# Kernel optimization log

Hardware: AMD Instinct MI355X
Metric: run time of the kernel (lower is better)

## Reference

```python
import jax, jax.numpy as jnp
import numpy as np

COST_CLASS, COST_BBOX, COST_GIOU = 1.0, 5.0, 2.0
BS, Q, K, T = 16, 1024, 256, 128


def setup_inputs() -> dict:
    key = jax.random.key(0)
    k1, k2, k3, k4 = jax.random.split(key, 4)
    pred_logits = jax.random.normal(k1, (BS, Q, K), dtype=jnp.float32)
    # predicted boxes in (mid, width) format, width > 0
    pred_boxes = jax.random.uniform(k2, (BS, Q, 2), dtype=jnp.float32, minval=0.05, maxval=1.0)
    # target boxes in (x0, x1) format with x0 < x1
    tgt_boxes = jnp.sort(jax.random.uniform(k3, (BS, T, 2), dtype=jnp.float32), axis=-1)
    tgt_labels = jax.random.randint(k4, (BS, T), 0, K, dtype=jnp.int32)
    return {"pred_logits": pred_logits, "pred_boxes": pred_boxes,
            "tgt_boxes": tgt_boxes, "tgt_labels": tgt_labels}


def midwtoxy(x):
    mid, w = x[..., 0], x[..., 1]
    return jnp.stack([mid - 0.5 * w, mid + 0.5 * w], axis=-1)


def getgiou(b1, b2):
    # b1: [N,2] (x0,x1), b2: [M,2]; returns [N,M] generalized IoU for 1-D intervals
    area1 = b1[:, 1] - b1[:, 0]              # [N]
    area2 = b2[:, 1] - b2[:, 0]              # [M]
    lt = jnp.maximum(b1[:, None, 0], b2[None, :, 0])
    rb = jnp.minimum(b1[:, None, 1], b2[None, :, 1])
    inter = jnp.clip(rb - lt, 0.0)           # [N,M]
    union = area1[:, None] + area2[None, :] - inter
    iou = inter / union
    hull_lt = jnp.minimum(b1[:, None, 0], b2[None, :, 0])
    hull_rb = jnp.maximum(b1[:, None, 1], b2[None, :, 1])
    hull = jnp.clip(hull_rb - hull_lt, 0.0)
    return iou - (hull - union) / hull


def reference(pred_logits, pred_boxes, tgt_boxes, tgt_labels):
    bs, q, k = pred_logits.shape
    out_prob = jax.nn.softmax(pred_logits.reshape(bs * q, k), axis=-1)  # [bs*Q, K]
    out_bbox = midwtoxy(pred_boxes.reshape(bs * q, 2))                  # [bs*Q, 2] (x0,x1)
    tgt_bbox = tgt_boxes.reshape(-1, 2)                                 # [bs*T, 2]
    tgt_ids = tgt_labels.reshape(-1)                                    # [bs*T]

    cost_class = -out_prob[:, tgt_ids]                                  # [bs*Q, bs*T]
    # L1 cdist over 2 coords, without materializing a [N,M,2] tensor
    cost_bbox = (jnp.abs(out_bbox[:, None, 0] - tgt_bbox[None, :, 0]) +
                 jnp.abs(out_bbox[:, None, 1] - tgt_bbox[None, :, 1]))
    cost_giou = -getgiou(out_bbox, tgt_bbox)

    C = COST_BBOX * cost_bbox + COST_CLASS * cost_class + COST_GIOU * cost_giou
    # [bs, Q, bs*T]; the original feeds the per-sample diagonal blocks
    # C[b, :, b*T:(b+1)*T] to scipy linear_sum_assignment (CPU, non-differentiable,
    # excluded from this GPU-math baseline).
    return C.reshape(bs, q, -1)
```

## Files before the change

kernel.cpp:

```cpp
#include <hip/hip_runtime.h>

#define BS 16
#define Q  1024
#define K  256
#define T  128
#define NROWS (BS * Q)
#define M     (BS * T)
#define RPB   16
#define TPB   512

typedef float f32x4 __attribute__((ext_vector_type(4)));

__device__ __forceinline__ float cost_fn(float x0, float x1, float hw1,
                                         float tx0, float tx1, float hw2,
                                         float p) {
    float d0   = x0 - tx0;
    float d1   = x1 - tx1;
    float l1   = fabsf(d0) + fabsf(d1);
    float hs   = hw1 + hw2;
    float ir   = fmaf(-0.5f, l1, hs);
    float hull = fmaf( 0.5f, l1, hs);
    float inter= fmaxf(ir, 0.0f);
    float mn   = fminf(ir, 0.0f);
    float uni  = hull + mn;
    float giou = (inter * hull + mn * uni) * __builtin_amdgcn_rcpf(uni * hull);
    return fmaf(5.0f, l1, -p) - 2.0f * giou;
}

__global__ __launch_bounds__(TPB, 8) void hungarian_cost_kernel(
    const float* __restrict__ pred_logits,
    const float* __restrict__ pred_boxes,
    const float* __restrict__ tgt_boxes,
    const int*   __restrict__ tgt_labels,
    float* __restrict__ out)
{
    __shared__ float probs[RPB][K];
    __shared__ float rboxs[RPB][3];

    const int t    = threadIdx.x;
    const int w    = t >> 6;
    const int lane = t & 63;
    const int row0 = blockIdx.x * RPB;

    const float4* tb4 = (const float4*)tgt_boxes;
    const int4*   tl4 = (const int4*)tgt_labels;
    float4 B01 = tb4[2 * t];
    float4 B23 = tb4[2 * t + 1];
    int4   LAB = tl4[t];

    if (t < RPB) {
        float2 mw = ((const float2*)pred_boxes)[row0 + t];
        rboxs[t][0] = mw.x - 0.5f * mw.y;
        rboxs[t][1] = mw.x + 0.5f * mw.y;
        rboxs[t][2] = 0.5f * mw.y;
    }

    #pragma unroll
    for (int r = 0; r < 2; ++r) {
        int lr = 2 * w + r;
        int n  = row0 + lr;
        float4 v = ((const float4*)(pred_logits + (size_t)n * K))[lane];
        float e0 = __expf(v.x), e1 = __expf(v.y), e2 = __expf(v.z), e3 = __expf(v.w);
        float sum = (e0 + e1) + (e2 + e3);
        #pragma unroll
        for (int off = 1; off < 64; off <<= 1)
            sum += __shfl_xor(sum, off, 64);
        float rs = __builtin_amdgcn_rcpf(sum);
        float4 pv; pv.x = e0 * rs; pv.y = e1 * rs; pv.z = e2 * rs; pv.w = e3 * rs;
        ((float4*)&probs[lr][0])[lane] = pv;
    }
    __syncthreads();

    float TX0[4], TX1[4], THW[4];
    TX0[0] = B01.x; TX1[0] = B01.y;
    TX0[1] = B01.z; TX1[1] = B01.w;
    TX0[2] = B23.x; TX1[2] = B23.y;
    TX0[3] = B23.z; TX1[3] = B23.w;
    #pragma unroll
    for (int j = 0; j < 4; ++j)
        THW[j] = 0.5f * (TX1[j] - TX0[j]);
    const float* lp0 = &probs[0][LAB.x];
    const float* lp1 = &probs[0][LAB.y];
    const float* lp2 = &probs[0][LAB.z];
    const float* lp3 = &probs[0][LAB.w];

    float* ob = out + (size_t)row0 * M;

    #pragma unroll
    for (int ch = 0; ch < 4; ++ch) {
        float pv[4][4];
        #pragma unroll
        for (int r = 0; r < 4; ++r) {
            int off = (ch * 4 + r) * K;
            pv[r][0] = lp0[off];
            pv[r][1] = lp1[off];
            pv[r][2] = lp2[off];
            pv[r][3] = lp3[off];
        }
        float rx0[4], rx1[4], rhw[4];
        #pragma unroll
        for (int r = 0; r < 4; ++r) {
            rx0[r] = rboxs[ch * 4 + r][0];
            rx1[r] = rboxs[ch * 4 + r][1];
            rhw[r] = rboxs[ch * 4 + r][2];
        }
        #pragma unroll
        for (int r = 0; r < 4; ++r) {
            f32x4 rr;
            rr.x = cost_fn(rx0[r], rx1[r], rhw[r], TX0[0], TX1[0], THW[0], pv[r][0]);
            rr.y = cost_fn(rx0[r], rx1[r], rhw[r], TX0[1], TX1[1], THW[1], pv[r][1]);
            rr.z = cost_fn(rx0[r], rx1[r], rhw[r], TX0[2], TX1[2], THW[2], pv[r][2]);
            rr.w = cost_fn(rx0[r], rx1[r], rhw[r], TX0[3], TX1[3], THW[3], pv[r][3]);
            __builtin_nontemporal_store(
                rr, ((f32x4*)(ob + (size_t)(ch * 4 + r) * M)) + t);
        }
    }
}

extern "C" void kernel_launch(void* const* d_in, const int* in_sizes, int n_in,
                              void* d_out, int out_size, void* d_ws, size_t ws_size,
                              hipStream_t stream) {
    const float* pred_logits = (const float*)d_in[0];
    const float* pred_boxes  = (const float*)d_in[1];
    const float* tgt_boxes   = (const float*)d_in[2];
    const int*   tgt_labels  = (const int*)d_in[3];
    float* out = (float*)d_out;

    hungarian_cost_kernel<<<NROWS / RPB, TPB, 0, stream>>>(
        pred_logits, pred_boxes, tgt_boxes, tgt_labels, out);
}
```

Baseline: 156.8 us.

## Split softmax into separate kernel via workspace and use plain stores

Unfuses the computation into a softmax kernel that writes probabilities to a workspace buffer and a cost kernel that copies a 16-row probability tile from global memory into shared memory. The intent is to shorten the cost kernel's prologue, so its output-writing phase starts sooner and overlaps better across blocks. It also swaps the nontemporal output stores for ordinary stores in both paths. The cost is an extra 16 MB written and read back plus a second launch. When no workspace is provided, it falls back to the fused kernel.

```diff
diff --git a/kernel.cpp b/kernel.cpp
--- a/kernel.cpp
+++ b/kernel.cpp
@@ -8,6 +8,7 @@
 #define M     (BS * T)
 #define RPB   16
 #define TPB   512
+
 
 typedef float f32x4 __attribute__((ext_vector_type(4)));
 
@@ -27,7 +28,109 @@
     return fmaf(5.0f, l1, -p) - 2.0f * giou;
 }
 
-__global__ __launch_bounds__(TPB, 8) void hungarian_cost_kernel(
+__global__ __launch_bounds__(256) void softmax_kernel(
+    const float* __restrict__ pred_logits,
+    float* __restrict__ probs_g)
+{
+    const int w    = threadIdx.x >> 6;
+    const int lane = threadIdx.x & 63;
+    const int row0 = blockIdx.x * 16 + w * 4;
+
+    #pragma unroll
+    for (int r = 0; r < 4; ++r) {
+        int n = row0 + r;
+        float4 v = ((const float4*)(pred_logits + (size_t)n * K))[lane];
+        float e0 = __expf(v.x), e1 = __expf(v.y), e2 = __expf(v.z), e3 = __expf(v.w);
+        float sum = (e0 + e1) + (e2 + e3);
+        #pragma unroll
+        for (int off = 1; off < 64; off <<= 1)
+            sum += __shfl_xor(sum, off, 64);
+        float rs = __builtin_amdgcn_rcpf(sum);
+        float4 pv; pv.x = e0 * rs; pv.y = e1 * rs; pv.z = e2 * rs; pv.w = e3 * rs;
+        ((float4*)(probs_g + (size_t)n * K))[lane] = pv;
+    }
+}
+
+__global__ __launch_bounds__(TPB, 8) void cost_kernel(
+    const float* __restrict__ probs_g,
+    const float* __restrict__ pred_boxes,
+    const float* __restrict__ tgt_boxes,
+    const int*   __restrict__ tgt_labels,
+    float* __restrict__ out)
+{
+    __shared__ float probs[RPB][K];
+    __shared__ float rboxs[RPB][3];
+
+    const int t    = threadIdx.x;
+    const int row0 = blockIdx.x * RPB;
+
+    const float4* tb4 = (const float4*)tgt_boxes;
+    const int4*   tl4 = (const int4*)tgt_labels;
+    float4 B01 = tb4[2 * t];
+    float4 B23 = tb4[2 * t + 1];
+    int4   LAB = tl4[t];
+
+    {
+        const float4* pg = (const float4*)(probs_g + (size_t)row0 * K);
+        float4* pl = (float4*)&probs[0][0];
+        pl[t]       = pg[t];
+        pl[t + 512] = pg[t + 512];
+    }
+
+    if (t < RPB) {
+        float2 mw = ((const float2*)pred_boxes)[row0 + t];
+        rboxs[t][0] = mw.x - 0.5f * mw.y;
+        rboxs[t][1] = mw.x + 0.5f * mw.y;
+        rboxs[t][2] = 0.5f * mw.y;
+    }
+    __syncthreads();
+
+    float TX0[4], TX1[4], THW[4];
+    TX0[0] = B01.x; TX1[0] = B01.y;
+    TX0[1] = B01.z; TX1[1] = B01.w;
+    TX0[2] = B23.x; TX1[2] = B23.y;
+    TX0[3] = B23.z; TX1[3] = B23.w;
+    #pragma unroll
+    for (int j = 0; j < 4; ++j)
+        THW[j] = 0.5f * (TX1[j] - TX0[j]);
+    const float* lp0 = &probs[0][LAB.x];
+    const float* lp1 = &probs[0][LAB.y];
+    const float* lp2 = &probs[0][LAB.z];
+    const float* lp3 = &probs[0][LAB.w];
+
+    float* ob = out + (size_t)row0 * M;
+
+    #pragma unroll
+    for (int ch = 0; ch < 4; ++ch) {
+        float pv[4][4];
+        #pragma unroll
+        for (int r = 0; r < 4; ++r) {
+            int off = (ch * 4 + r) * K;
+            pv[r][0] = lp0[off];
+            pv[r][1] = lp1[off];
+            pv[r][2] = lp2[off];
+            pv[r][3] = lp3[off];
+        }
+        float rx0[4], rx1[4], rhw[4];
+        #pragma unroll
+        for (int r = 0; r < 4; ++r) {
+            rx0[r] = rboxs[ch * 4 + r][0];
+            rx1[r] = rboxs[ch * 4 + r][1];
+            rhw[r] = rboxs[ch * 4 + r][2];
+        }
+        #pragma unroll
+        for (int r = 0; r < 4; ++r) {
+            f32x4 rr;
+            rr.x = cost_fn(rx0[r], rx1[r], rhw[r], TX0[0], TX1[0], THW[0], pv[r][0]);
+            rr.y = cost_fn(rx0[r], rx1[r], rhw[r], TX0[1], TX1[1], THW[1], pv[r][1]);
+            rr.z = cost_fn(rx0[r], rx1[r], rhw[r], TX0[2], TX1[2], THW[2], pv[r][2]);
+            rr.w = cost_fn(rx0[r], rx1[r], rhw[r], TX0[3], TX1[3], THW[3], pv[r][3]);
+            *(((f32x4*)(ob + (size_t)(ch * 4 + r) * M)) + t) = rr;
+        }
+    }
+}
+
+__global__ __launch_bounds__(TPB, 8) void fused_kernel(
     const float* __restrict__ pred_logits,
     const float* __restrict__ pred_boxes,
     const float* __restrict__ tgt_boxes,
@@ -111,8 +214,7 @@
             rr.y = cost_fn(rx0[r], rx1[r], rhw[r], TX0[1], TX1[1], THW[1], pv[r][1]);
             rr.z = cost_fn(rx0[r], rx1[r], rhw[r], TX0[2], TX1[2], THW[2], pv[r][2]);
             rr.w = cost_fn(rx0[r], rx1[r], rhw[r], TX0[3], TX1[3], THW[3], pv[r][3]);
-            __builtin_nontemporal_store(
-                rr, ((f32x4*)(ob + (size_t)(ch * 4 + r) * M)) + t);
+            *(((f32x4*)(ob + (size_t)(ch * 4 + r) * M)) + t) = rr;
         }
     }
 }
@@ -126,6 +228,14 @@
     const int*   tgt_labels  = (const int*)d_in[3];
     float* out = (float*)d_out;
 
-    hungarian_cost_kernel<<<NROWS / RPB, TPB, 0, stream>>>(
-        pred_logits, pred_boxes, tgt_boxes, tgt_labels, out);
-}
+    const size_t probs_bytes = (size_t)NROWS * K * sizeof(float);
+    if (d_ws != nullptr && ws_size >= probs_bytes) {
+        float* probs_g = (float*)d_ws;
+        softmax_kernel<<<NROWS / 16, 256, 0, stream>>>(pred_logits, probs_g);
+        cost_kernel<<<NROWS / RPB, TPB, 0, stream>>>(
+            probs_g, pred_boxes, tgt_boxes, tgt_labels, out);
+    } else {
+        fused_kernel<<<NROWS / RPB, TPB, 0, stream>>>(
+            pred_logits, pred_boxes, tgt_boxes, tgt_labels, out);
+    }
+}
```

New measurement: 154.9 us. No clear change (-1.2%).
